# Performance work log

Measured on AMD Instinct MI355X. Metric: run time of the kernel, lower is better.

Reference implementation:

```python
import jax, jax.numpy as jnp
import numpy as np

B, N, C = 2, 2048, 1024
H = 16
D = C // H  # head dim = 64


def setup_inputs() -> dict:
    key = jax.random.key(0)
    ks = jax.random.split(key, 11)
    s = 1.0 / np.sqrt(C)
    inp = {
        "q": jax.random.normal(ks[0], (B, N, C), jnp.float32),
        "k": jax.random.normal(ks[1], (B, N, C), jnp.float32),
        "v": jax.random.normal(ks[2], (B, N, C), jnp.float32),
        # Linear params (kernel shape [in, out], as in flax)
        "Wq": jax.random.normal(ks[3], (C, C), jnp.float32) * s,
        "bq": jnp.zeros((C,), jnp.float32),
        "Wk": jax.random.normal(ks[4], (C, C), jnp.float32) * s,
        "bk": jnp.zeros((C,), jnp.float32),
        "Wv": jax.random.normal(ks[5], (C, C), jnp.float32) * s,
        "bv": jnp.zeros((C,), jnp.float32),
        "Wo": jax.random.normal(ks[6], (C, C), jnp.float32) * s,
        "bo": jnp.zeros((C,), jnp.float32),
    }
    return inp


def reference(q, k, v, Wq, bq, Wk, bk, Wv, bv, Wo, bo):
    # QKV projections: (B,N,C) @ (C,C) + bias
    qh = (q @ Wq + bq).reshape(B, N, H, D).transpose(0, 2, 1, 3)  # b h n d
    kh = (k @ Wk + bk).reshape(B, N, H, D).transpose(0, 2, 1, 3)
    vh = (v @ Wv + bv).reshape(B, N, H, D).transpose(0, 2, 1, 3)
    scale = 1.0 / np.sqrt(D)
    attn = jnp.einsum('bhqd,bhkd->bhqk', qh * scale, kh)  # full NxN scores
    attn = jax.nn.softmax(attn, axis=-1)
    out = jnp.einsum('bhqk,bhkd->bhqd', attn, vh)
    out = out.transpose(0, 2, 1, 3).reshape(B, N, C)
    return out @ Wo + bo
```

## Files before the change

kernel.cpp:

```cpp
#include <hip/hip_runtime.h>
#include <hip/hip_bf16.h>
#include <math.h>


typedef __attribute__((ext_vector_type(8))) short bf16x8;
typedef __attribute__((ext_vector_type(4))) short bf16x4;
typedef __attribute__((ext_vector_type(4))) float f32x4;
typedef __attribute__((ext_vector_type(2))) unsigned int u32x2;

__device__ __forceinline__ short f2bf(float f) {
    union { float f; unsigned u; } x; x.f = f;
    unsigned r = x.u + 0x7fffu + ((x.u >> 16) & 1u);
    return (short)(r >> 16);
}

__device__ __forceinline__ unsigned cvt_pk_bf16(float lo, float hi) {
    unsigned r;
    asm volatile("v_cvt_pk_bf16_f32 %0, %1, %2" : "=v"(r) : "v"(lo), "v"(hi));
    return r;
}

__global__ __launch_bounds__(256) void prep_w(const float* __restrict__ Wq,
                                              const float* __restrict__ Wk,
                                              const float* __restrict__ Wv,
                                              const float* __restrict__ Wo,
                                              short* __restrict__ wt) {
    __shared__ float tile[32][33];
    const float* W = blockIdx.z == 0 ? Wq : blockIdx.z == 1 ? Wk
                   : blockIdx.z == 2 ? Wv : Wo;
    short* dst = wt + (size_t)blockIdx.z * 1048576;
    const int bx = blockIdx.x * 32, by = blockIdx.y * 32;
    const int tx = threadIdx.x & 31, ty = threadIdx.x >> 5;
#pragma unroll
    for (int i = 0; i < 32; i += 8)
        tile[ty + i][tx] = W[(size_t)(by + ty + i) * 1024 + bx + tx];
    __syncthreads();
#pragma unroll
    for (int i = 0; i < 32; i += 8)
        dst[(size_t)(bx + ty + i) * 1024 + by + tx] = f2bf(tile[tx][ty + i]);
}

__global__ __launch_bounds__(256) void gemm_qkv(const float* __restrict__ qA,
                                                const float* __restrict__ kA,
                                                const float* __restrict__ vA,
                                                const short* __restrict__ wt,
                                                const float* __restrict__ bq,
                                                const float* __restrict__ bk,
                                                const float* __restrict__ bv,
                                                short* __restrict__ qh,
                                                short* __restrict__ khp,
                                                short* __restrict__ vtp,
                                                float qscale) {
    __shared__ short As[128 * 32];
    __shared__ short Bs[64 * 32];
    const int tid = threadIdx.x;
    const int l = tid & 63, w = tid >> 6;
    const int wr = w >> 1, wc = w & 1;
    const int row16 = l & 15, lg = l >> 4;
    const int m0 = blockIdx.x * 128;
    const int n0 = blockIdx.y * 64;
    const int z = blockIdx.z;

    const float* A = z == 0 ? qA : z == 1 ? kA : vA;
    const short* Wt = wt + (size_t)z * 1048576;
    const float* bias = z == 0 ? bq : z == 1 ? bk : bv;
    const float scale = z == 0 ? qscale : 1.0f;
    short* outp = z == 0 ? qh : z == 1 ? khp : vtp;

    const int ar = tid >> 1, ac = (tid & 1) * 16;
    const int br = tid >> 2, bc = (tid & 3) * 8;

    f32x4 acc[4][2] = {};

    f32x4 x0, x1, x2, x3; bf16x8 bfrag;
    {
        const float* src = A + (size_t)(m0 + ar) * 1024 + ac;
        x0 = ((const f32x4*)src)[0]; x1 = ((const f32x4*)src)[1];
        x2 = ((const f32x4*)src)[2]; x3 = ((const f32x4*)src)[3];
        bfrag = *(const bf16x8*)(Wt + (size_t)(n0 + br) * 1024 + bc);
    }

    for (int t = 0; t < 32; ++t) {
        __syncthreads();
        bf16x8 sa0, sa1;
#pragma unroll
        for (int j = 0; j < 4; ++j) {
            sa0[j] = f2bf(x0[j]); sa0[4 + j] = f2bf(x1[j]);
            sa1[j] = f2bf(x2[j]); sa1[4 + j] = f2bf(x3[j]);
        }
        *(bf16x8*)&As[ar * 32 + ac]     = sa0;
        *(bf16x8*)&As[ar * 32 + ac + 8] = sa1;
        *(bf16x8*)&Bs[br * 32 + bc]     = bfrag;
        __syncthreads();
        if (t < 31) {
            const int k0 = (t + 1) * 32;
            const float* src = A + (size_t)(m0 + ar) * 1024 + k0 + ac;
            x0 = ((const f32x4*)src)[0]; x1 = ((const f32x4*)src)[1];
            x2 = ((const f32x4*)src)[2]; x3 = ((const f32x4*)src)[3];
            bfrag = *(const bf16x8*)(Wt + (size_t)(n0 + br) * 1024 + k0 + bc);
        }
        bf16x8 af[4], bf2[2];
#pragma unroll
        for (int m = 0; m < 4; ++m)
            af[m] = *(const bf16x8*)&As[(wr * 64 + m * 16 + row16) * 32 + lg * 8];
#pragma unroll
        for (int n = 0; n < 2; ++n)
            bf2[n] = *(const bf16x8*)&Bs[(wc * 32 + n * 16 + row16) * 32 + lg * 8];
#pragma unroll
        for (int m = 0; m < 4; ++m)
#pragma unroll
            for (int n = 0; n < 2; ++n)
                acc[m][n] = __builtin_amdgcn_mfma_f32_16x16x32_bf16(af[m], bf2[n], acc[m][n], 0, 0, 0);
    }

#pragma unroll
    for (int n = 0; n < 2; ++n) {
        const int col = n0 + wc * 32 + n * 16 + row16;
        const float bvl = bias[col];
        const int h = col >> 6, d = col & 63;
#pragma unroll
        for (int m = 0; m < 4; ++m) {
#pragma unroll
            for (int r = 0; r < 4; ++r) {
                const int row = m0 + wr * 64 + m * 16 + lg * 4 + r;
                const float val = (acc[m][n][r] + bvl) * scale;
                const int b = row >> 11, nt = row & 2047;
                if (z != 2)
                    outp[(((size_t)(b * 16 + h)) * 2048 + nt) * 64 + d] = f2bf(val);
                else
                    outp[(((size_t)(b * 16 + h)) * 64 + d) * 2048 + nt] = f2bf(val);
            }
        }
    }
}

__global__ __launch_bounds__(256) void gemm_out(const short* __restrict__ Ab,
                                                const short* __restrict__ Wt,
                                                const float* __restrict__ bias,
                                                float* __restrict__ outp) {
    __shared__ short As[128 * 32];
    __shared__ short Bs[64 * 32];
    const int tid = threadIdx.x;
    const int l = tid & 63, w = tid >> 6;
    const int wr = w >> 1, wc = w & 1;
    const int row16 = l & 15, lg = l >> 4;
    const int m0 = blockIdx.x * 128;
    const int n0 = blockIdx.y * 64;

    const int ar = tid >> 1, ac = (tid & 1) * 16;
    const int br = tid >> 2, bc = (tid & 3) * 8;

    f32x4 acc[4][2] = {};

    bf16x8 sa0, sa1, bfrag;
    sa0 = *(const bf16x8*)(Ab + (size_t)(m0 + ar) * 1024 + ac);
    sa1 = *(const bf16x8*)(Ab + (size_t)(m0 + ar) * 1024 + ac + 8);
    bfrag = *(const bf16x8*)(Wt + (size_t)(n0 + br) * 1024 + bc);

    for (int t = 0; t < 32; ++t) {
        __syncthreads();
        *(bf16x8*)&As[ar * 32 + ac]     = sa0;
        *(bf16x8*)&As[ar * 32 + ac + 8] = sa1;
        *(bf16x8*)&Bs[br * 32 + bc]     = bfrag;
        __syncthreads();
        if (t < 31) {
            const int k0 = (t + 1) * 32;
            sa0 = *(const bf16x8*)(Ab + (size_t)(m0 + ar) * 1024 + k0 + ac);
            sa1 = *(const bf16x8*)(Ab + (size_t)(m0 + ar) * 1024 + k0 + ac + 8);
            bfrag = *(const bf16x8*)(Wt + (size_t)(n0 + br) * 1024 + k0 + bc);
        }
        bf16x8 af[4], bf2[2];
#pragma unroll
        for (int m = 0; m < 4; ++m)
            af[m] = *(const bf16x8*)&As[(wr * 64 + m * 16 + row16) * 32 + lg * 8];
#pragma unroll
        for (int n = 0; n < 2; ++n)
            bf2[n] = *(const bf16x8*)&Bs[(wc * 32 + n * 16 + row16) * 32 + lg * 8];
#pragma unroll
        for (int m = 0; m < 4; ++m)
#pragma unroll
            for (int n = 0; n < 2; ++n)
                acc[m][n] = __builtin_amdgcn_mfma_f32_16x16x32_bf16(af[m], bf2[n], acc[m][n], 0, 0, 0);
    }

#pragma unroll
    for (int n = 0; n < 2; ++n) {
        const int col = n0 + wc * 32 + n * 16 + row16;
        const float bvl = bias[col];
#pragma unroll
        for (int m = 0; m < 4; ++m) {
#pragma unroll
            for (int r = 0; r < 4; ++r) {
                const int row = m0 + wr * 64 + m * 16 + lg * 4 + r;
                outp[(size_t)row * 1024 + col] = acc[m][n][r] + bvl;
            }
        }
    }
}

__global__ __launch_bounds__(256) void attn_kernel(const short* __restrict__ qh,
                                                   const short* __restrict__ kh,
                                                   const short* __restrict__ vt,
                                                   short* __restrict__ aout) {
    __shared__ short Pls[8][16 * 72];

    const int tid = threadIdx.x;
    const int l = tid & 63, w = tid >> 6;
    const int row16 = l & 15, lg = l >> 4;
    const int bh = blockIdx.y;
    const int q0 = blockIdx.x * 128 + w * 32;

    const short* kbase = kh + (size_t)bh * 2048 * 64;
    const short* vbase = vt + (size_t)bh * 64 * 2048;

    bf16x8 qf[2][2];
#pragma unroll
    for (int qt = 0; qt < 2; ++qt)
#pragma unroll
        for (int kk = 0; kk < 2; ++kk)
            qf[qt][kk] = *(const bf16x8*)&qh[((size_t)bh * 2048 + q0 + qt * 16 + row16) * 64 + kk * 32 + lg * 8];

    bf16x8 ones;
#pragma unroll
    for (int j = 0; j < 8; ++j) ones[j] = (short)0x3F80;

    f32x4 oac[2][4] = {};
    f32x4 lacc[2] = {};

    short* prow0 = &Pls[w * 2 + 0][row16 * 72];
    short* prow1 = &Pls[w * 2 + 1][row16 * 72];
    short* prow[2] = {prow0, prow1};

    bf16x8 kf[4][2], vf[4][2], pf[2][2];
#pragma unroll
    for (int kt = 0; kt < 4; ++kt)
#pragma unroll
        for (int kk = 0; kk < 2; ++kk) {
            kf[kt][kk] = *(const bf16x8*)&kbase[(size_t)(kt * 16 + row16) * 64 + kk * 32 + lg * 8];
            vf[kt][kk] = *(const bf16x8*)&vbase[(size_t)(kt * 16 + row16) * 2048 + kk * 32 + lg * 8];
        }

    {
        f32x4 s[2][4] = {};
#pragma unroll
        for (int kt = 0; kt < 4; ++kt)
#pragma unroll
            for (int kk = 0; kk < 2; ++kk) {
                s[0][kt] = __builtin_amdgcn_mfma_f32_16x16x32_bf16(kf[kt][kk], qf[0][kk], s[0][kt], 0, 0, 0);
                s[1][kt] = __builtin_amdgcn_mfma_f32_16x16x32_bf16(kf[kt][kk], qf[1][kk], s[1][kt], 0, 0, 0);
            }
#pragma unroll
        for (int kt = 0; kt < 4; ++kt)
#pragma unroll
            for (int kk = 0; kk < 2; ++kk)
                kf[kt][kk] = *(const bf16x8*)&kbase[(size_t)(64 + kt * 16 + row16) * 64 + kk * 32 + lg * 8];
#pragma unroll
        for (int qt = 0; qt < 2; ++qt)
#pragma unroll
            for (int kt = 0; kt < 4; ++kt) {
                u32x2 pk;
                pk.x = cvt_pk_bf16(exp2f(s[qt][kt][0]), exp2f(s[qt][kt][1]));
                pk.y = cvt_pk_bf16(exp2f(s[qt][kt][2]), exp2f(s[qt][kt][3]));
                *(u32x2*)&prow[qt][kt * 16 + lg * 4] = pk;
            }
        asm volatile("s_waitcnt lgkmcnt(0)" ::: "memory");
#pragma unroll
        for (int qt = 0; qt < 2; ++qt)
#pragma unroll
            for (int kk = 0; kk < 2; ++kk)
                pf[qt][kk] = *(const bf16x8*)&prow[qt][kk * 32 + lg * 8];
        asm volatile("" ::: "memory");
    }

    for (int t = 1; t < 32; ++t) {
        const int kvn = t * 64;
        const int kvnn = ((t + 1) & 31) * 64;

        f32x4 s[2][4] = {};
#pragma unroll
        for (int kt = 0; kt < 4; ++kt)
#pragma unroll
            for (int kk = 0; kk < 2; ++kk) {
                s[0][kt] = __builtin_amdgcn_mfma_f32_16x16x32_bf16(kf[kt][kk], qf[0][kk], s[0][kt], 0, 0, 0);
                s[1][kt] = __builtin_amdgcn_mfma_f32_16x16x32_bf16(kf[kt][kk], qf[1][kk], s[1][kt], 0, 0, 0);
            }
#pragma unroll
        for (int kt = 0; kt < 4; ++kt)
#pragma unroll
            for (int kk = 0; kk < 2; ++kk)
                kf[kt][kk] = *(const bf16x8*)&kbase[(size_t)(kvnn + kt * 16 + row16) * 64 + kk * 32 + lg * 8];

#pragma unroll
        for (int qt = 0; qt < 2; ++qt)
#pragma unroll
            for (int kt = 0; kt < 4; ++kt) {
                u32x2 pk;
                pk.x = cvt_pk_bf16(exp2f(s[qt][kt][0]), exp2f(s[qt][kt][1]));
                pk.y = cvt_pk_bf16(exp2f(s[qt][kt][2]), exp2f(s[qt][kt][3]));
                *(u32x2*)&prow[qt][kt * 16 + lg * 4] = pk;
            }

#pragma unroll
        for (int dt = 0; dt < 4; ++dt)
#pragma unroll
            for (int kk = 0; kk < 2; ++kk) {
                oac[0][dt] = __builtin_amdgcn_mfma_f32_16x16x32_bf16(pf[0][kk], vf[dt][kk], oac[0][dt], 0, 0, 0);
                oac[1][dt] = __builtin_amdgcn_mfma_f32_16x16x32_bf16(pf[1][kk], vf[dt][kk], oac[1][dt], 0, 0, 0);
            }
#pragma unroll
        for (int qt = 0; qt < 2; ++qt)
#pragma unroll
            for (int kk = 0; kk < 2; ++kk)
                lacc[qt] = __builtin_amdgcn_mfma_f32_16x16x32_bf16(pf[qt][kk], ones, lacc[qt], 0, 0, 0);

#pragma unroll
        for (int dt = 0; dt < 4; ++dt)
#pragma unroll
            for (int kk = 0; kk < 2; ++kk)
                vf[dt][kk] = *(const bf16x8*)&vbase[(size_t)(dt * 16 + row16) * 2048 + kvn + kk * 32 + lg * 8];

        asm volatile("s_waitcnt lgkmcnt(0)" ::: "memory");
#pragma unroll
        for (int qt = 0; qt < 2; ++qt)
#pragma unroll
            for (int kk = 0; kk < 2; ++kk)
                pf[qt][kk] = *(const bf16x8*)&prow[qt][kk * 32 + lg * 8];
        asm volatile("" ::: "memory");
    }

#pragma unroll
    for (int dt = 0; dt < 4; ++dt)
#pragma unroll
        for (int kk = 0; kk < 2; ++kk) {
            oac[0][dt] = __builtin_amdgcn_mfma_f32_16x16x32_bf16(pf[0][kk], vf[dt][kk], oac[0][dt], 0, 0, 0);
            oac[1][dt] = __builtin_amdgcn_mfma_f32_16x16x32_bf16(pf[1][kk], vf[dt][kk], oac[1][dt], 0, 0, 0);
        }
#pragma unroll
    for (int qt = 0; qt < 2; ++qt)
#pragma unroll
        for (int kk = 0; kk < 2; ++kk)
            lacc[qt] = __builtin_amdgcn_mfma_f32_16x16x32_bf16(pf[qt][kk], ones, lacc[qt], 0, 0, 0);

    const int b = bh >> 4, h = bh & 15;
#pragma unroll
    for (int qt = 0; qt < 2; ++qt) {
#pragma unroll
        for (int r = 0; r < 4; ++r) {
            const float iv = 1.f / lacc[qt][r];
            const int qrow = q0 + qt * 16 + lg * 4 + r;
#pragma unroll
            for (int dt = 0; dt < 4; ++dt) {
                const int c = h * 64 + dt * 16 + row16;
                aout[((size_t)b * 2048 + qrow) * 1024 + c] = f2bf(oac[qt][dt][r] * iv);
            }
        }
    }
}

extern "C" void kernel_launch(void* const* d_in, const int* in_sizes, int n_in,
                              void* d_out, int out_size, void* d_ws, size_t ws_size,
                              hipStream_t stream) {
    const float* q  = (const float*)d_in[0];
    const float* k  = (const float*)d_in[1];
    const float* v  = (const float*)d_in[2];
    const float* Wq = (const float*)d_in[3];
    const float* bq = (const float*)d_in[4];
    const float* Wk = (const float*)d_in[5];
    const float* bk = (const float*)d_in[6];
    const float* Wv = (const float*)d_in[7];
    const float* bv = (const float*)d_in[8];
    const float* Wo = (const float*)d_in[9];
    const float* bo = (const float*)d_in[10];

    char* ws = (char*)d_ws;
    short* wt   = (short*)ws;
    short* qh   = (short*)(ws + (8u  << 20));
    short* khp  = (short*)(ws + (16u << 20));
    short* vt   = (short*)(ws + (24u << 20));
    short* aout = (short*)(ws + (32u << 20));

    const float qscale = 0.125f * 1.44269504088896340736f;

    prep_w<<<dim3(32, 32, 4), 256, 0, stream>>>(Wq, Wk, Wv, Wo, wt);
    gemm_qkv<<<dim3(32, 16, 3), 256, 0, stream>>>(q, k, v, wt, bq, bk, bv,
                                                  qh, khp, vt, qscale);
    attn_kernel<<<dim3(16, 32), 256, 0, stream>>>(qh, khp, vt, aout);
    gemm_out<<<dim3(32, 16), 256, 0, stream>>>(aout, wt + 3145728, bo, (float*)d_out);
}
```

Measured before the change: 221.0 us.

## Double-buffer K fragments two tiles ahead and remap blocks across XCDs

K register fragments are now prefetched two iterations ahead using ping-pong buffers (kfA/kfB). The main loop is unrolled by two through a helper step function so more global-load latency is hidden behind the MFMA work. The block-to-(head, query-tile) mapping is also changed so all query tiles of a head land on the same XCD, which should improve L2 reuse of K/V. The extra K buffers raise register pressure and could lower occupancy.

```diff
diff --git a/kernel.cpp b/kernel.cpp
--- a/kernel.cpp
+++ b/kernel.cpp
@@ -198,6 +198,72 @@
     }
 }
 
+__device__ __forceinline__ void attn_step(int t,
+                                          const short* __restrict__ kbase,
+                                          const short* __restrict__ vbase,
+                                          bf16x8 (&kc)[4][2],
+                                          bf16x8 (&vf)[4][2],
+                                          bf16x8 (&qf)[2][2], bf16x8 (&pf)[2][2],
+                                          f32x4 (&oac)[2][4], f32x4 (&lacc)[2],
+                                          const bf16x8& ones,
+                                          short* prow0, short* prow1,
+                                          int row16, int lg) {
+    const int kvn = t * 64;
+    const int kvp = ((t + 2) & 31) * 64;
+    short* prow[2] = {prow0, prow1};
+
+    f32x4 s[2][4] = {};
+#pragma unroll
+    for (int kt = 0; kt < 4; ++kt)
+#pragma unroll
+        for (int kk = 0; kk < 2; ++kk) {
+            s[0][kt] = __builtin_amdgcn_mfma_f32_16x16x32_bf16(kc[kt][kk], qf[0][kk], s[0][kt], 0, 0, 0);
+            s[1][kt] = __builtin_amdgcn_mfma_f32_16x16x32_bf16(kc[kt][kk], qf[1][kk], s[1][kt], 0, 0, 0);
+        }
+#pragma unroll
+    for (int kt = 0; kt < 4; ++kt)
+#pragma unroll
+        for (int kk = 0; kk < 2; ++kk)
+            kc[kt][kk] = *(const bf16x8*)&kbase[(size_t)(kvp + kt * 16 + row16) * 64 + kk * 32 + lg * 8];
+
+#pragma unroll
+    for (int qt = 0; qt < 2; ++qt)
+#pragma unroll
+        for (int kt = 0; kt < 4; ++kt) {
+            u32x2 pk;
+            pk.x = cvt_pk_bf16(exp2f(s[qt][kt][0]), exp2f(s[qt][kt][1]));
+            pk.y = cvt_pk_bf16(exp2f(s[qt][kt][2]), exp2f(s[qt][kt][3]));
+            *(u32x2*)&prow[qt][kt * 16 + lg * 4] = pk;
+        }
+
+#pragma unroll
+    for (int dt = 0; dt < 4; ++dt)
+#pragma unroll
+        for (int kk = 0; kk < 2; ++kk) {
+            oac[0][dt] = __builtin_amdgcn_mfma_f32_16x16x32_bf16(pf[0][kk], vf[dt][kk], oac[0][dt], 0, 0, 0);
+            oac[1][dt] = __builtin_amdgcn_mfma_f32_16x16x32_bf16(pf[1][kk], vf[dt][kk], oac[1][dt], 0, 0, 0);
+        }
+#pragma unroll
+    for (int qt = 0; qt < 2; ++qt)
+#pragma unroll
+        for (int kk = 0; kk < 2; ++kk)
+            lacc[qt] = __builtin_amdgcn_mfma_f32_16x16x32_bf16(pf[qt][kk], ones, lacc[qt], 0, 0, 0);
+
+#pragma unroll
+    for (int dt = 0; dt < 4; ++dt)
+#pragma unroll
+        for (int kk = 0; kk < 2; ++kk)
+            vf[dt][kk] = *(const bf16x8*)&vbase[(size_t)(dt * 16 + row16) * 2048 + kvn + kk * 32 + lg * 8];
+
+    asm volatile("s_waitcnt lgkmcnt(0)" ::: "memory");
+#pragma unroll
+    for (int qt = 0; qt < 2; ++qt)
+#pragma unroll
+        for (int kk = 0; kk < 2; ++kk)
+            pf[qt][kk] = *(const bf16x8*)&prow[qt][kk * 32 + lg * 8];
+    asm volatile("" ::: "memory");
+}
+
 __global__ __launch_bounds__(256) void attn_kernel(const short* __restrict__ qh,
                                                    const short* __restrict__ kh,
                                                    const short* __restrict__ vt,
@@ -207,8 +273,11 @@
     const int tid = threadIdx.x;
     const int l = tid & 63, w = tid >> 6;
     const int row16 = l & 15, lg = l >> 4;
-    const int bh = blockIdx.y;
-    const int q0 = blockIdx.x * 128 + w * 32;
+
+    const int fid = blockIdx.y * 16 + blockIdx.x;
+    const int xcd = fid & 7, slot = fid >> 3;
+    const int bh = xcd * 4 + (slot >> 4);
+    const int q0 = (slot & 15) * 128 + w * 32;
 
     const short* kbase = kh + (size_t)bh * 2048 * 64;
     const short* vbase = vt + (size_t)bh * 64 * 2048;
@@ -231,13 +300,14 @@
     short* prow1 = &Pls[w * 2 + 1][row16 * 72];
     short* prow[2] = {prow0, prow1};
 
-    bf16x8 kf[4][2], vf[4][2], pf[2][2];
+    bf16x8 kfA[4][2], kfB[4][2], vf[4][2], pf[2][2];
 #pragma unroll
     for (int kt = 0; kt < 4; ++kt)
 #pragma unroll
         for (int kk = 0; kk < 2; ++kk) {
-            kf[kt][kk] = *(const bf16x8*)&kbase[(size_t)(kt * 16 + row16) * 64 + kk * 32 + lg * 8];
-            vf[kt][kk] = *(const bf16x8*)&vbase[(size_t)(kt * 16 + row16) * 2048 + kk * 32 + lg * 8];
+            kfA[kt][kk] = *(const bf16x8*)&kbase[(size_t)(kt * 16 + row16) * 64 + kk * 32 + lg * 8];
+            kfB[kt][kk] = *(const bf16x8*)&kbase[(size_t)(64 + kt * 16 + row16) * 64 + kk * 32 + lg * 8];
+            vf[kt][kk]  = *(const bf16x8*)&vbase[(size_t)(kt * 16 + row16) * 2048 + kk * 32 + lg * 8];
         }
 
     {
@@ -246,14 +316,14 @@
         for (int kt = 0; kt < 4; ++kt)
 #pragma unroll
             for (int kk = 0; kk < 2; ++kk) {
-                s[0][kt] = __builtin_amdgcn_mfma_f32_16x16x32_bf16(kf[kt][kk], qf[0][kk], s[0][kt], 0, 0, 0);
-                s[1][kt] = __builtin_amdgcn_mfma_f32_16x16x32_bf16(kf[kt][kk], qf[1][kk], s[1][kt], 0, 0, 0);
+                s[0][kt] = __builtin_amdgcn_mfma_f32_16x16x32_bf16(kfA[kt][kk], qf[0][kk], s[0][kt], 0, 0, 0);
+                s[1][kt] = __builtin_amdgcn_mfma_f32_16x16x32_bf16(kfA[kt][kk], qf[1][kk], s[1][kt], 0, 0, 0);
             }
 #pragma unroll
         for (int kt = 0; kt < 4; ++kt)
 #pragma unroll
             for (int kk = 0; kk < 2; ++kk)
-                kf[kt][kk] = *(const bf16x8*)&kbase[(size_t)(64 + kt * 16 + row16) * 64 + kk * 32 + lg * 8];
+                kfA[kt][kk] = *(const bf16x8*)&kbase[(size_t)(128 + kt * 16 + row16) * 64 + kk * 32 + lg * 8];
 #pragma unroll
         for (int qt = 0; qt < 2; ++qt)
 #pragma unroll
@@ -272,61 +342,11 @@
         asm volatile("" ::: "memory");
     }
 
-    for (int t = 1; t < 32; ++t) {
-        const int kvn = t * 64;
-        const int kvnn = ((t + 1) & 31) * 64;
-
-        f32x4 s[2][4] = {};
-#pragma unroll
-        for (int kt = 0; kt < 4; ++kt)
-#pragma unroll
-            for (int kk = 0; kk < 2; ++kk) {
-                s[0][kt] = __builtin_amdgcn_mfma_f32_16x16x32_bf16(kf[kt][kk], qf[0][kk], s[0][kt], 0, 0, 0);
-                s[1][kt] = __builtin_amdgcn_mfma_f32_16x16x32_bf16(kf[kt][kk], qf[1][kk], s[1][kt], 0, 0, 0);
-            }
-#pragma unroll
-        for (int kt = 0; kt < 4; ++kt)
-#pragma unroll
-            for (int kk = 0; kk < 2; ++kk)
-                kf[kt][kk] = *(const bf16x8*)&kbase[(size_t)(kvnn + kt * 16 + row16) * 64 + kk * 32 + lg * 8];
-
-#pragma unroll
-        for (int qt = 0; qt < 2; ++qt)
-#pragma unroll
-            for (int kt = 0; kt < 4; ++kt) {
-                u32x2 pk;
-                pk.x = cvt_pk_bf16(exp2f(s[qt][kt][0]), exp2f(s[qt][kt][1]));
-                pk.y = cvt_pk_bf16(exp2f(s[qt][kt][2]), exp2f(s[qt][kt][3]));
-                *(u32x2*)&prow[qt][kt * 16 + lg * 4] = pk;
-            }
-
-#pragma unroll
-        for (int dt = 0; dt < 4; ++dt)
-#pragma unroll
-            for (int kk = 0; kk < 2; ++kk) {
-                oac[0][dt] = __builtin_amdgcn_mfma_f32_16x16x32_bf16(pf[0][kk], vf[dt][kk], oac[0][dt], 0, 0, 0);
-                oac[1][dt] = __builtin_amdgcn_mfma_f32_16x16x32_bf16(pf[1][kk], vf[dt][kk], oac[1][dt], 0, 0, 0);
-            }
-#pragma unroll
-        for (int qt = 0; qt < 2; ++qt)
-#pragma unroll
-            for (int kk = 0; kk < 2; ++kk)
-                lacc[qt] = __builtin_amdgcn_mfma_f32_16x16x32_bf16(pf[qt][kk], ones, lacc[qt], 0, 0, 0);
-
-#pragma unroll
-        for (int dt = 0; dt < 4; ++dt)
-#pragma unroll
-            for (int kk = 0; kk < 2; ++kk)
-                vf[dt][kk] = *(const bf16x8*)&vbase[(size_t)(dt * 16 + row16) * 2048 + kvn + kk * 32 + lg * 8];
-
-        asm volatile("s_waitcnt lgkmcnt(0)" ::: "memory");
-#pragma unroll
-        for (int qt = 0; qt < 2; ++qt)
-#pragma unroll
-            for (int kk = 0; kk < 2; ++kk)
-                pf[qt][kk] = *(const bf16x8*)&prow[qt][kk * 32 + lg * 8];
-        asm volatile("" ::: "memory");
-    }
+    for (int tt = 1; tt < 31; tt += 2) {
+        attn_step(tt,     kbase, vbase, kfB, vf, qf, pf, oac, lacc, ones, prow0, prow1, row16, lg);
+        attn_step(tt + 1, kbase, vbase, kfA, vf, qf, pf, oac, lacc, ones, prow0, prow1, row16, lg);
+    }
+    attn_step(31, kbase, vbase, kfB, vf, qf, pf, oac, lacc, ones, prow0, prow1, row16, lg);
 
 #pragma unroll
     for (int dt = 0; dt < 4; ++dt)
```

Result: no change. 220.4 us (-0.3%).
